# Kernel tuning notes

Measured on AMD Instinct MI355X. Metric: run time of the kernel, lower is better.

Reference implementation:

```python
import jax, jax.numpy as jnp
import numpy as np

S, T, N, D, H, DT = 4, 4, 65536, 128, 128, 128


def setup_inputs() -> dict:
    key = jax.random.key(0)
    ks = jax.random.split(key, 9)
    inv_d = 1.0 / np.sqrt(D)
    inv_h = 1.0 / np.sqrt(H)
    return {
        "states": jax.random.normal(ks[0], (N, D), dtype=jnp.float32),
        "scores": jax.random.uniform(ks[1], (N, 1), dtype=jnp.float32),
        "type_ids": jax.random.randint(ks[2], (N,), 0, S, dtype=jnp.int32),
        "type_matching": jax.random.normal(ks[3], (S, T), dtype=jnp.float32),
        "W1": jax.random.normal(ks[4], (S, T, D, H), dtype=jnp.float32) * inv_d,
        "b1": jnp.zeros((S, T, H), dtype=jnp.float32),
        "W2": jax.random.normal(ks[5], (S, T, H, DT), dtype=jnp.float32) * inv_h,
        "b2": jnp.zeros((S, T, DT), dtype=jnp.float32),
        "C1": jax.random.normal(ks[6], (S, T, D, H), dtype=jnp.float32) * inv_d,
        "c1": jnp.zeros((S, T, H), dtype=jnp.float32),
        "C2": jax.random.normal(ks[7], (S, T, H, 1), dtype=jnp.float32) * inv_h,
        "c2": jnp.zeros((S, T, 1), dtype=jnp.float32),
    }


def reference(states, scores, type_ids, type_matching, W1, b1, W2, b2, C1, c1, C2, c2):
    """Batched MetaphorMorphism.forward with best_match_only=True.

    For each item with source type s: route to t* = argmax sigmoid(type_matching[s]),
    apply mapper MLP (D->H->DT, ReLU), classifier MLP (D->H->1, ReLU, sigmoid),
    new_score = min(score, classifier_out), item_prob = sigmoid(type_matching)[s, t*].
    """
    match_sig = jax.nn.sigmoid(type_matching)          # [S, T]
    best_t = jnp.argmax(type_matching, axis=1)         # [S] (argmax of sigmoid == argmax of logits)
    best_prob = match_sig[jnp.arange(S), best_t]       # [S]

    out_state = jnp.zeros((states.shape[0], W2.shape[-1]), dtype=states.dtype)
    out_score = jnp.zeros_like(scores)
    # loop over the small, fixed set of source types (structurally distinct experts)
    for s in range(S):
        t = best_t[s]
        h = jax.nn.relu(states @ W1[s, t] + b1[s, t])          # [N, H]
        y = h @ W2[s, t] + b2[s, t]                            # [N, DT]
        hc = jax.nn.relu(states @ C1[s, t] + c1[s, t])         # [N, H]
        cls = jax.nn.sigmoid(hc @ C2[s, t] + c2[s, t])         # [N, 1]
        new_score = jnp.minimum(scores, cls)                   # [N, 1]
        m = (type_ids == s)[:, None]
        out_state = jnp.where(m, y, out_state)
        out_score = jnp.where(m, new_score, out_score)
    item_prob = best_prob[type_ids]                            # [N]
    return out_state, out_score, item_prob
```

## Files before the change

### kernel.cpp

```cpp
#include <hip/hip_runtime.h>
#include <hip/hip_bf16.h>

#define Nn 65536

typedef short s16x8 __attribute__((ext_vector_type(8)));
typedef float f32x4 __attribute__((ext_vector_type(4)));

__device__ __forceinline__ unsigned short f2bf(float x) {
    unsigned int u = __float_as_uint(x);
    u += 0x7FFFu + ((u >> 16) & 1u);
    return (unsigned short)(u >> 16);
}

__device__ __forceinline__ int best_t_for(const float* __restrict__ tm, int s, float* mOut) {
    float m = tm[s * 4];
    int am = 0;
    #pragma unroll
    for (int j = 1; j < 4; ++j) {
        float v = tm[s * 4 + j];
        if (v > m) { m = v; am = j; }
    }
    if (mOut) *mOut = m;
    return am;
}

__global__ void k_count(const int* __restrict__ type_ids, const float* __restrict__ tm,
                        int* __restrict__ blockHist, float* __restrict__ out_prob) {
    __shared__ float prob[4];
    __shared__ int hist[4];
    const int tid = threadIdx.x;
    if (tid < 4) {
        hist[tid] = 0;
        float m;
        best_t_for(tm, tid, &m);
        prob[tid] = 1.f / (1.f + expf(-m));
    }
    __syncthreads();
    const int gid = blockIdx.x * 256 + tid;
    int4 ids = ((const int4*)type_ids)[gid];
    float4 p;
    p.x = prob[ids.x]; p.y = prob[ids.y]; p.z = prob[ids.z]; p.w = prob[ids.w];
    ((float4*)out_prob)[gid] = p;
    const int lane = tid & 63;
    int idarr[4] = {ids.x, ids.y, ids.z, ids.w};
    #pragma unroll
    for (int j = 0; j < 4; ++j) {
        #pragma unroll
        for (int sv = 0; sv < 4; ++sv) {
            unsigned long long m = __ballot(idarr[j] == sv);
            if (lane == 0 && m) atomicAdd(&hist[sv], __popcll(m));
        }
    }
    __syncthreads();
    if (tid < 4) blockHist[blockIdx.x * 4 + tid] = hist[tid];
}

__global__ void k_scatter(const int* __restrict__ type_ids, const int* __restrict__ blockHist,
                          int* __restrict__ buckets, int* __restrict__ counts) {
    __shared__ int histAll[256];
    __shared__ int off[4];
    const int tid = threadIdx.x;
    histAll[tid] = blockHist[tid];
    __syncthreads();
    if (tid < 4) {
        int ex = 0, tot = 0;
        for (int b = 0; b < 64; ++b) {
            int v = histAll[b * 4 + tid];
            if (b < (int)blockIdx.x) ex += v;
            tot += v;
        }
        off[tid] = ex;
        if (blockIdx.x == 0) counts[tid] = tot;
    }
    __syncthreads();
    const int gid = blockIdx.x * 256 + tid;
    int4 ids = ((const int4*)type_ids)[gid];
    const int base = gid * 4;
    int idarr[4] = {ids.x, ids.y, ids.z, ids.w};
    #pragma unroll
    for (int j = 0; j < 4; ++j) {
        int sv = idarr[j];
        int pos = atomicAdd(&off[sv], 1);
        buckets[sv * Nn + pos] = base + j;
    }
}

__global__ void k_convert(const float* __restrict__ W1, const float* __restrict__ W2,
                          const float* __restrict__ C1, const float* __restrict__ tm,
                          unsigned short* __restrict__ wbf) {
    int idx = blockIdx.x * 256 + threadIdx.x;
    int mat = idx >> 14;
    int e = idx & 16383;
    int s = mat / 3, w = mat % 3;
    int t = best_t_for(tm, s, nullptr);
    int row = e >> 7, col = e & 127;
    const float* src = (w == 0) ? W1 : (w == 1) ? W2 : C1;
    float v = src[((s * 4 + t) << 14) + col * 128 + row];
    wbf[idx] = f2bf(v);
}

__global__ __launch_bounds__(256, 2) void k_main(
    const float* __restrict__ states, const float* __restrict__ scores,
    const float* __restrict__ b1g, const float* __restrict__ b2g, const float* __restrict__ c1g,
    const float* __restrict__ tm, const float* __restrict__ C2, const float* __restrict__ c2,
    const int* __restrict__ counts, const int* __restrict__ buckets,
    const unsigned short* __restrict__ wbf,
    float* __restrict__ out_state, float* __restrict__ out_score)
{
    __shared__ int gIdx[64];
    __shared__ float C2s[128];
    __shared__ unsigned short Abuf[64 * 136];
    __shared__ unsigned short Hbuf[64 * 136];
    __shared__ unsigned short Wbuf[128 * 136];

    const int s = blockIdx.y;
    const int cnt = counts[s];
    const int rowBase = blockIdx.x << 6;
    if (rowBase >= cnt) return;
    const int valid = (cnt - rowBase < 64) ? (cnt - rowBase) : 64;
    const int t = threadIdx.x;
    const int tt = best_t_for(tm, s, nullptr);
    const int stIdx = s * 4 + tt;

    if (t < 64) gIdx[t] = (t < valid) ? buckets[s * Nn + rowBase + t] : -1;
    if (t >= 128 && t < 256) C2s[t - 128] = C2[stIdx * 128 + (t - 128)];
    __syncthreads();

    {
        int r = t >> 2, q = t & 3;
        int g = gIdx[r];
        unsigned short* dst = &Abuf[r * 136 + q * 32];
        if (g >= 0) {
            const float4* src = (const float4*)(states + (size_t)g * 128 + q * 32);
            #pragma unroll
            for (int i = 0; i < 8; ++i) {
                float4 v = src[i];
                ushort4 o;
                o.x = f2bf(v.x); o.y = f2bf(v.y); o.z = f2bf(v.z); o.w = f2bf(v.w);
                *(ushort4*)(dst + i * 4) = o;
            }
        } else {
            #pragma unroll
            for (int i = 0; i < 8; ++i) *(ushort4*)(dst + i * 4) = ushort4{0, 0, 0, 0};
        }
    }

    const int lane = t & 63;
    const int wv = t >> 6;
    const int m0 = wv << 4;
    const int l15 = lane & 15;
    const int quad = lane >> 4;
    const int kq = quad << 3;

    auto stageW = [&](const unsigned short* src) {
        #pragma unroll
        for (int i = 0; i < 8; ++i) {
            int idx = (t + i * 256) * 8;
            int row = idx >> 7, col = idx & 127;
            s16x8 v = *(const s16x8*)(src + idx);
            *(s16x8*)(&Wbuf[row * 136 + col]) = v;
        }
    };

    auto gemm = [&](const unsigned short* Ab, f32x4 acc[8]) {
        #pragma unroll
        for (int n = 0; n < 8; ++n) acc[n] = f32x4{0.f, 0.f, 0.f, 0.f};
        #pragma unroll
        for (int kk = 0; kk < 4; ++kk) {
            s16x8 af = *(const s16x8*)(Ab + (m0 + l15) * 136 + kk * 32 + kq);
            #pragma unroll
            for (int n = 0; n < 8; ++n) {
                s16x8 bf = *(const s16x8*)(&Wbuf[(n * 16 + l15) * 136 + kk * 32 + kq]);
                acc[n] = __builtin_amdgcn_mfma_f32_16x16x32_bf16(af, bf, acc[n], 0, 0, 0);
            }
        }
    };

    f32x4 acc[8];

    stageW(wbf + (s * 3 + 0) * 16384);
    __syncthreads();
    gemm(Abuf, acc);
    {
        const float* b1p = b1g + stIdx * 128;
        #pragma unroll
        for (int n = 0; n < 8; ++n) {
            int col = n * 16 + l15;
            float bias = b1p[col];
            #pragma unroll
            for (int r = 0; r < 4; ++r) {
                float v = fmaxf(acc[n][r] + bias, 0.f);
                Hbuf[(m0 + quad * 4 + r) * 136 + col] = f2bf(v);
            }
        }
    }
    __syncthreads();

    stageW(wbf + (s * 3 + 1) * 16384);
    __syncthreads();
    gemm(Hbuf, acc);
    {
        int grow[4];
        #pragma unroll
        for (int r = 0; r < 4; ++r) {
            int row = m0 + quad * 4 + r;
            grow[r] = (row < valid) ? gIdx[row] : -1;
        }
        const float* b2p = b2g + stIdx * 128;
        #pragma unroll
        for (int n = 0; n < 8; ++n) {
            int col = n * 16 + l15;
            float bias = b2p[col];
            #pragma unroll
            for (int r = 0; r < 4; ++r) {
                if (grow[r] >= 0) out_state[(size_t)grow[r] * 128 + col] = acc[n][r] + bias;
            }
        }
    }
    __syncthreads();

    stageW(wbf + (s * 3 + 2) * 16384);
    __syncthreads();
    gemm(Abuf, acc);
    {
        const float* c1p = c1g + stIdx * 128;
        float part[4] = {0.f, 0.f, 0.f, 0.f};
        #pragma unroll
        for (int n = 0; n < 8; ++n) {
            int col = n * 16 + l15;
            float cb = c1p[col];
            float cw = C2s[col];
            #pragma unroll
            for (int r = 0; r < 4; ++r) {
                float v = fmaxf(acc[n][r] + cb, 0.f);
                part[r] += v * cw;
            }
        }
        #pragma unroll
        for (int off = 1; off < 16; off <<= 1) {
            #pragma unroll
            for (int r = 0; r < 4; ++r) part[r] += __shfl_xor(part[r], off, 64);
        }
        if (l15 == 0) {
            float c2s = c2[stIdx];
            #pragma unroll
            for (int r = 0; r < 4; ++r) {
                int row = m0 + quad * 4 + r;
                if (row < valid) {
                    int g = gIdx[row];
                    float cls = 1.f / (1.f + expf(-(part[r] + c2s)));
                    out_score[g] = fminf(scores[g], cls);
                }
            }
        }
    }
}

extern "C" void kernel_launch(void* const* d_in, const int* in_sizes, int n_in,
                              void* d_out, int out_size, void* d_ws, size_t ws_size,
                              hipStream_t stream) {
    const float* states = (const float*)d_in[0];
    const float* scores = (const float*)d_in[1];
    const int*   type_ids = (const int*)d_in[2];
    const float* tm = (const float*)d_in[3];
    const float* W1 = (const float*)d_in[4];
    const float* b1 = (const float*)d_in[5];
    const float* W2 = (const float*)d_in[6];
    const float* b2 = (const float*)d_in[7];
    const float* C1 = (const float*)d_in[8];
    const float* c1 = (const float*)d_in[9];
    const float* C2 = (const float*)d_in[10];
    const float* c2 = (const float*)d_in[11];

    char* ws = (char*)d_ws;
    int*   counts    = (int*)(ws + 0);
    int*   blockHist = (int*)(ws + 64);
    int*   buckets   = (int*)(ws + 4096);
    unsigned short* wbf = (unsigned short*)(ws + 1052672);

    float* out_state = (float*)d_out;
    float* out_score = out_state + (size_t)Nn * 128;
    float* out_prob  = out_score + Nn;

    k_count<<<64, 256, 0, stream>>>(type_ids, tm, blockHist, out_prob);
    k_scatter<<<64, 256, 0, stream>>>(type_ids, blockHist, buckets, counts);
    k_convert<<<768, 256, 0, stream>>>(W1, W2, C1, tm, wbf);
    k_main<<<dim3(1024, 4), 256, 0, stream>>>(states, scores, b1, b2, c1,
        tm, C2, c2, counts, buckets, wbf, out_state, out_score);
}
```

Measured before the change: 143.3 us.

## Fuse prep kernels and make main kernel persistent with resident weights and prefetch

```diff
diff --git a/kernel.cpp b/kernel.cpp
--- a/kernel.cpp
+++ b/kernel.cpp
@@ -1,13 +1,14 @@
 #include <hip/hip_runtime.h>
-#include <hip/hip_bf16.h>
+#include <math.h>
 
 #define Nn 65536
 
 typedef short s16x8 __attribute__((ext_vector_type(8)));
 typedef float f32x4 __attribute__((ext_vector_type(4)));
+typedef unsigned int u32;
 
 __device__ __forceinline__ unsigned short f2bf(float x) {
-    unsigned int u = __float_as_uint(x);
+    u32 u = __float_as_uint(x);
     u += 0x7FFFu + ((u >> 16) & 1u);
     return (unsigned short)(u >> 16);
 }
@@ -15,7 +16,7 @@
 __device__ __forceinline__ int best_t_for(const float* __restrict__ tm, int s, float* mOut) {
     float m = tm[s * 4];
     int am = 0;
-    #pragma unroll
+#pragma unroll
     for (int j = 1; j < 4; ++j) {
         float v = tm[s * 4 + j];
         if (v > m) { m = v; am = j; }
@@ -24,82 +25,72 @@
     return am;
 }
 
-__global__ void k_count(const int* __restrict__ type_ids, const float* __restrict__ tm,
-                        int* __restrict__ blockHist, float* __restrict__ out_prob) {
-    __shared__ float prob[4];
-    __shared__ int hist[4];
+#define GLDS16(g, l) __builtin_amdgcn_global_load_lds( \
+    (const __attribute__((address_space(1))) u32*)(g), \
+    (__attribute__((address_space(3))) u32*)(l), 16, 0, 0)
+
+__global__ void k_prep(const int* __restrict__ type_ids, const float* __restrict__ tm,
+                       const float* __restrict__ W1, const float* __restrict__ W2,
+                       const float* __restrict__ C1,
+                       int* __restrict__ counts, int* __restrict__ buckets,
+                       unsigned short* __restrict__ wbf, float* __restrict__ out_prob) {
     const int tid = threadIdx.x;
-    if (tid < 4) {
-        hist[tid] = 0;
-        float m;
-        best_t_for(tm, tid, &m);
-        prob[tid] = 1.f / (1.f + expf(-m));
-    }
-    __syncthreads();
-    const int gid = blockIdx.x * 256 + tid;
-    int4 ids = ((const int4*)type_ids)[gid];
-    float4 p;
-    p.x = prob[ids.x]; p.y = prob[ids.y]; p.z = prob[ids.z]; p.w = prob[ids.w];
-    ((float4*)out_prob)[gid] = p;
-    const int lane = tid & 63;
-    int idarr[4] = {ids.x, ids.y, ids.z, ids.w};
-    #pragma unroll
-    for (int j = 0; j < 4; ++j) {
-        #pragma unroll
-        for (int sv = 0; sv < 4; ++sv) {
-            unsigned long long m = __ballot(idarr[j] == sv);
-            if (lane == 0 && m) atomicAdd(&hist[sv], __popcll(m));
-        }
-    }
-    __syncthreads();
-    if (tid < 4) blockHist[blockIdx.x * 4 + tid] = hist[tid];
-}
-
-__global__ void k_scatter(const int* __restrict__ type_ids, const int* __restrict__ blockHist,
-                          int* __restrict__ buckets, int* __restrict__ counts) {
-    __shared__ int histAll[256];
-    __shared__ int off[4];
-    const int tid = threadIdx.x;
-    histAll[tid] = blockHist[tid];
-    __syncthreads();
-    if (tid < 4) {
-        int ex = 0, tot = 0;
-        for (int b = 0; b < 64; ++b) {
-            int v = histAll[b * 4 + tid];
-            if (b < (int)blockIdx.x) ex += v;
-            tot += v;
-        }
-        off[tid] = ex;
-        if (blockIdx.x == 0) counts[tid] = tot;
-    }
-    __syncthreads();
-    const int gid = blockIdx.x * 256 + tid;
-    int4 ids = ((const int4*)type_ids)[gid];
-    const int base = gid * 4;
-    int idarr[4] = {ids.x, ids.y, ids.z, ids.w};
-    #pragma unroll
-    for (int j = 0; j < 4; ++j) {
-        int sv = idarr[j];
-        int pos = atomicAdd(&off[sv], 1);
-        buckets[sv * Nn + pos] = base + j;
-    }
-}
-
-__global__ void k_convert(const float* __restrict__ W1, const float* __restrict__ W2,
-                          const float* __restrict__ C1, const float* __restrict__ tm,
-                          unsigned short* __restrict__ wbf) {
-    int idx = blockIdx.x * 256 + threadIdx.x;
-    int mat = idx >> 14;
-    int e = idx & 16383;
-    int s = mat / 3, w = mat % 3;
-    int t = best_t_for(tm, s, nullptr);
-    int row = e >> 7, col = e & 127;
-    const float* src = (w == 0) ? W1 : (w == 1) ? W2 : C1;
-    float v = src[((s * 4 + t) << 14) + col * 128 + row];
-    wbf[idx] = f2bf(v);
-}
-
-__global__ __launch_bounds__(256, 2) void k_main(
+    if (blockIdx.x < 64) {
+        __shared__ int hist[4];
+        __shared__ int off[4];
+        __shared__ float prob[4];
+        if (tid < 4) {
+            hist[tid] = 0;
+            float m;
+            best_t_for(tm, tid, &m);
+            prob[tid] = 1.f / (1.f + expf(-m));
+        }
+        __syncthreads();
+        const int gid = blockIdx.x * 256 + tid;
+        int4 ids = ((const int4*)type_ids)[gid];
+        float4 p;
+        p.x = prob[ids.x]; p.y = prob[ids.y]; p.z = prob[ids.z]; p.w = prob[ids.w];
+        ((float4*)out_prob)[gid] = p;
+        const int lane = tid & 63;
+        int idarr[4] = {ids.x, ids.y, ids.z, ids.w};
+#pragma unroll
+        for (int j = 0; j < 4; ++j) {
+#pragma unroll
+            for (int sv = 0; sv < 4; ++sv) {
+                unsigned long long m = __ballot(idarr[j] == sv);
+                if (lane == 0 && m) atomicAdd(&hist[sv], __popcll(m));
+            }
+        }
+        __syncthreads();
+        if (tid < 4) off[tid] = atomicAdd(&counts[tid], hist[tid]);
+        __syncthreads();
+        const int base = gid * 4;
+#pragma unroll
+        for (int j = 0; j < 4; ++j) {
+            int sv = idarr[j];
+            int pos = atomicAdd(&off[sv], 1);
+            buckets[sv * Nn + pos] = base + j;
+        }
+    } else {
+        int u = (blockIdx.x - 64) * 256 + tid;
+        int mat = u >> 11;
+        int rr = u & 2047;
+        int f = rr >> 6, lane = rr & 63;
+        int kk = f >> 3, n8 = f & 7;
+        int q = lane >> 4, l15 = lane & 15;
+        int sm = mat / 3, w = mat - sm * 3;
+        int t = best_t_for(tm, sm, nullptr);
+        const float* src = (w == 0) ? W1 : (w == 1) ? W2 : C1;
+        const float* sp = src + (((sm * 4 + t) << 14) + n8 * 16 + l15);
+        int k0 = kk * 32 + q * 8;
+        s16x8 o;
+#pragma unroll
+        for (int j = 0; j < 8; ++j) o[j] = (short)f2bf(sp[(k0 + j) * 128]);
+        *(s16x8*)(wbf + (size_t)u * 8) = o;
+    }
+}
+
+__global__ __launch_bounds__(256, 1) void k_main(
     const float* __restrict__ states, const float* __restrict__ scores,
     const float* __restrict__ b1g, const float* __restrict__ b2g, const float* __restrict__ c1g,
     const float* __restrict__ tm, const float* __restrict__ C2, const float* __restrict__ c2,
@@ -107,152 +98,185 @@
     const unsigned short* __restrict__ wbf,
     float* __restrict__ out_state, float* __restrict__ out_score)
 {
-    __shared__ int gIdx[64];
+    __shared__ unsigned short Wlds[3 * 16384];
+    __shared__ unsigned short Abuf[2][64 * 136];
+    __shared__ unsigned short Hbuf[64 * 136];
+    __shared__ int gIdxLds[2][64];
     __shared__ float C2s[128];
-    __shared__ unsigned short Abuf[64 * 136];
-    __shared__ unsigned short Hbuf[64 * 136];
-    __shared__ unsigned short Wbuf[128 * 136];
 
     const int s = blockIdx.y;
+    const int bx = blockIdx.x;
     const int cnt = counts[s];
-    const int rowBase = blockIdx.x << 6;
-    if (rowBase >= cnt) return;
-    const int valid = (cnt - rowBase < 64) ? (cnt - rowBase) : 64;
+    const int ntiles = (cnt + 63) >> 6;
+    if (bx >= ntiles) return;
     const int t = threadIdx.x;
     const int tt = best_t_for(tm, s, nullptr);
     const int stIdx = s * 4 + tt;
 
-    if (t < 64) gIdx[t] = (t < valid) ? buckets[s * Nn + rowBase + t] : -1;
-    if (t >= 128 && t < 256) C2s[t - 128] = C2[stIdx * 128 + (t - 128)];
-    __syncthreads();
-
     {
-        int r = t >> 2, q = t & 3;
-        int g = gIdx[r];
-        unsigned short* dst = &Abuf[r * 136 + q * 32];
-        if (g >= 0) {
-            const float4* src = (const float4*)(states + (size_t)g * 128 + q * 32);
-            #pragma unroll
-            for (int i = 0; i < 8; ++i) {
-                float4 v = src[i];
-                ushort4 o;
-                o.x = f2bf(v.x); o.y = f2bf(v.y); o.z = f2bf(v.z); o.w = f2bf(v.w);
-                *(ushort4*)(dst + i * 4) = o;
-            }
-        } else {
-            #pragma unroll
-            for (int i = 0; i < 8; ++i) *(ushort4*)(dst + i * 4) = ushort4{0, 0, 0, 0};
-        }
-    }
+        const unsigned short* src = wbf + (size_t)s * 3 * 16384;
+#pragma unroll
+        for (int i = 0; i < 24; ++i) {
+            GLDS16(src + t * 8 + i * 2048, Wlds + t * 8 + i * 2048);
+        }
+    }
+    if (t >= 128) C2s[t - 128] = C2[stIdx * 128 + (t - 128)];
 
     const int lane = t & 63;
-    const int wv = t >> 6;
-    const int m0 = wv << 4;
+    const int m0 = (t >> 6) << 4;
     const int l15 = lane & 15;
     const int quad = lane >> 4;
     const int kq = quad << 3;
-
-    auto stageW = [&](const unsigned short* src) {
-        #pragma unroll
-        for (int i = 0; i < 8; ++i) {
-            int idx = (t + i * 256) * 8;
-            int row = idx >> 7, col = idx & 127;
-            s16x8 v = *(const s16x8*)(src + idx);
-            *(s16x8*)(&Wbuf[row * 136 + col]) = v;
-        }
-    };
-
-    auto gemm = [&](const unsigned short* Ab, f32x4 acc[8]) {
-        #pragma unroll
+    const int myRow = t >> 2;
+    const int q4 = t & 3;
+
+    const int* bkt = buckets + s * Nn;
+
+    {
+        int gr = bx * 64 + myRow;
+        int rIdxC = (gr < cnt) ? bkt[gr] : -1;
+        if ((t & 3) == 0) gIdxLds[0][myRow] = rIdxC;
+        unsigned short* dst = &Abuf[0][myRow * 136 + q4 * 32];
+        if (rIdxC >= 0) {
+            const float4* sp = (const float4*)(states + (size_t)rIdxC * 128 + q4 * 32);
+            float4 pf0[8];
+#pragma unroll
+            for (int i = 0; i < 8; ++i) pf0[i] = sp[i];
+#pragma unroll
+            for (int i = 0; i < 8; ++i) {
+                ushort4 o;
+                o.x = f2bf(pf0[i].x); o.y = f2bf(pf0[i].y);
+                o.z = f2bf(pf0[i].z); o.w = f2bf(pf0[i].w);
+                *(ushort4*)(dst + i * 4) = o;
+            }
+        } else {
+#pragma unroll
+            for (int i = 0; i < 8; ++i) *(ushort4*)(dst + i * 4) = ushort4{0, 0, 0, 0};
+        }
+    }
+    int rIdxN = -1;
+    if (bx + 64 < ntiles) {
+        int gr = (bx + 64) * 64 + myRow;
+        rIdxN = (gr < cnt) ? bkt[gr] : -1;
+    }
+    __syncthreads();
+
+    auto gemm = [&](const unsigned short* Ab, const unsigned short* Wm, f32x4 acc[8]) {
+#pragma unroll
         for (int n = 0; n < 8; ++n) acc[n] = f32x4{0.f, 0.f, 0.f, 0.f};
-        #pragma unroll
+#pragma unroll
         for (int kk = 0; kk < 4; ++kk) {
             s16x8 af = *(const s16x8*)(Ab + (m0 + l15) * 136 + kk * 32 + kq);
-            #pragma unroll
+#pragma unroll
             for (int n = 0; n < 8; ++n) {
-                s16x8 bf = *(const s16x8*)(&Wbuf[(n * 16 + l15) * 136 + kk * 32 + kq]);
+                s16x8 bf = *(const s16x8*)(Wm + (size_t)((kk * 8 + n) * 64 + lane) * 8);
                 acc[n] = __builtin_amdgcn_mfma_f32_16x16x32_bf16(af, bf, acc[n], 0, 0, 0);
             }
         }
     };
 
     f32x4 acc[8];
-
-    stageW(wbf + (s * 3 + 0) * 16384);
-    __syncthreads();
-    gemm(Abuf, acc);
-    {
-        const float* b1p = b1g + stIdx * 128;
-        #pragma unroll
-        for (int n = 0; n < 8; ++n) {
-            int col = n * 16 + l15;
-            float bias = b1p[col];
-            #pragma unroll
-            for (int r = 0; r < 4; ++r) {
-                float v = fmaxf(acc[n][r] + bias, 0.f);
-                Hbuf[(m0 + quad * 4 + r) * 136 + col] = f2bf(v);
-            }
-        }
-    }
-    __syncthreads();
-
-    stageW(wbf + (s * 3 + 1) * 16384);
-    __syncthreads();
-    gemm(Hbuf, acc);
-    {
-        int grow[4];
-        #pragma unroll
-        for (int r = 0; r < 4; ++r) {
-            int row = m0 + quad * 4 + r;
-            grow[r] = (row < valid) ? gIdx[row] : -1;
-        }
-        const float* b2p = b2g + stIdx * 128;
-        #pragma unroll
-        for (int n = 0; n < 8; ++n) {
-            int col = n * 16 + l15;
-            float bias = b2p[col];
-            #pragma unroll
-            for (int r = 0; r < 4; ++r) {
-                if (grow[r] >= 0) out_state[(size_t)grow[r] * 128 + col] = acc[n][r] + bias;
-            }
-        }
-    }
-    __syncthreads();
-
-    stageW(wbf + (s * 3 + 2) * 16384);
-    __syncthreads();
-    gemm(Abuf, acc);
-    {
-        const float* c1p = c1g + stIdx * 128;
-        float part[4] = {0.f, 0.f, 0.f, 0.f};
-        #pragma unroll
-        for (int n = 0; n < 8; ++n) {
-            int col = n * 16 + l15;
-            float cb = c1p[col];
-            float cw = C2s[col];
-            #pragma unroll
-            for (int r = 0; r < 4; ++r) {
-                float v = fmaxf(acc[n][r] + cb, 0.f);
-                part[r] += v * cw;
-            }
-        }
-        #pragma unroll
-        for (int off = 1; off < 16; off <<= 1) {
-            #pragma unroll
-            for (int r = 0; r < 4; ++r) part[r] += __shfl_xor(part[r], off, 64);
-        }
-        if (l15 == 0) {
-            float c2s = c2[stIdx];
-            #pragma unroll
-            for (int r = 0; r < 4; ++r) {
-                int row = m0 + quad * 4 + r;
-                if (row < valid) {
-                    int g = gIdx[row];
-                    float cls = 1.f / (1.f + expf(-(part[r] + c2s)));
-                    out_score[g] = fminf(scores[g], cls);
-                }
-            }
-        }
+    int cur = 0;
+    for (int tile = bx; tile < ntiles; tile += 64, cur ^= 1) {
+        const int nxt = cur ^ 1;
+        const bool hasNext = (tile + 64) < ntiles;
+
+        gemm(Abuf[cur], Wlds, acc);
+        {
+            const float* b1p = b1g + stIdx * 128;
+#pragma unroll
+            for (int n = 0; n < 8; ++n) {
+                int col = n * 16 + l15;
+                float bias = b1p[col];
+#pragma unroll
+                for (int r = 0; r < 4; ++r) {
+                    float v = fmaxf(acc[n][r] + bias, 0.f);
+                    Hbuf[(m0 + quad * 4 + r) * 136 + col] = f2bf(v);
+                }
+            }
+        }
+        if ((t & 3) == 0) gIdxLds[nxt][myRow] = rIdxN;
+        __syncthreads();
+
+        float4 pf[8];
+        if (hasNext && rIdxN >= 0) {
+            const float4* sp = (const float4*)(states + (size_t)rIdxN * 128 + q4 * 32);
+#pragma unroll
+            for (int i = 0; i < 8; ++i) pf[i] = sp[i];
+        }
+        int rIdxN2 = -1;
+        if (tile + 128 < ntiles) {
+            int gr = (tile + 128) * 64 + myRow;
+            rIdxN2 = (gr < cnt) ? bkt[gr] : -1;
+        }
+
+        gemm(Hbuf, Wlds + 16384, acc);
+        {
+            const float* b2p = b2g + stIdx * 128;
+            int grow[4];
+#pragma unroll
+            for (int r = 0; r < 4; ++r) grow[r] = gIdxLds[cur][m0 + quad * 4 + r];
+#pragma unroll
+            for (int n = 0; n < 8; ++n) {
+                int col = n * 16 + l15;
+                float bias = b2p[col];
+#pragma unroll
+                for (int r = 0; r < 4; ++r) {
+                    if (grow[r] >= 0) out_state[(size_t)grow[r] * 128 + col] = acc[n][r] + bias;
+                }
+            }
+        }
+
+        gemm(Abuf[cur], Wlds + 2 * 16384, acc);
+        {
+            const float* c1p = c1g + stIdx * 128;
+            float part[4] = {0.f, 0.f, 0.f, 0.f};
+#pragma unroll
+            for (int n = 0; n < 8; ++n) {
+                int col = n * 16 + l15;
+                float cb = c1p[col];
+                float cw = C2s[col];
+#pragma unroll
+                for (int r = 0; r < 4; ++r) {
+                    float v = fmaxf(acc[n][r] + cb, 0.f);
+                    part[r] += v * cw;
+                }
+            }
+#pragma unroll
+            for (int off = 1; off < 16; off <<= 1) {
+#pragma unroll
+                for (int r = 0; r < 4; ++r) part[r] += __shfl_xor(part[r], off, 64);
+            }
+            if (l15 == 0) {
+                float c2s = c2[stIdx];
+#pragma unroll
+                for (int r = 0; r < 4; ++r) {
+                    int g = gIdxLds[cur][m0 + quad * 4 + r];
+                    if (g >= 0) {
+                        float cls = 1.f / (1.f + expf(-(part[r] + c2s)));
+                        out_score[g] = fminf(scores[g], cls);
+                    }
+                }
+            }
+        }
+
+        if (hasNext) {
+            unsigned short* dst = &Abuf[nxt][myRow * 136 + q4 * 32];
+            if (rIdxN >= 0) {
+#pragma unroll
+                for (int i = 0; i < 8; ++i) {
+                    ushort4 o;
+                    o.x = f2bf(pf[i].x); o.y = f2bf(pf[i].y);
+                    o.z = f2bf(pf[i].z); o.w = f2bf(pf[i].w);
+                    *(ushort4*)(dst + i * 4) = o;
+                }
+            } else {
+#pragma unroll
+                for (int i = 0; i < 8; ++i) *(ushort4*)(dst + i * 4) = ushort4{0, 0, 0, 0};
+            }
+        }
+        rIdxN = rIdxN2;
+        __syncthreads();
     }
 }
 
@@ -273,18 +297,16 @@
     const float* c2 = (const float*)d_in[11];
 
     char* ws = (char*)d_ws;
-    int*   counts    = (int*)(ws + 0);
-    int*   blockHist = (int*)(ws + 64);
-    int*   buckets   = (int*)(ws + 4096);
+    int*   counts  = (int*)(ws + 0);
+    int*   buckets = (int*)(ws + 4096);
     unsigned short* wbf = (unsigned short*)(ws + 1052672);
 
     float* out_state = (float*)d_out;
     float* out_score = out_state + (size_t)Nn * 128;
     float* out_prob  = out_score + Nn;
 
-    k_count<<<64, 256, 0, stream>>>(type_ids, tm, blockHist, out_prob);
-    k_scatter<<<64, 256, 0, stream>>>(type_ids, blockHist, buckets, counts);
-    k_convert<<<768, 256, 0, stream>>>(W1, W2, C1, tm, wbf);
-    k_main<<<dim3(1024, 4), 256, 0, stream>>>(states, scores, b1, b2, c1,
+    hipMemsetAsync(counts, 0, 16, stream);
+    k_prep<<<160, 256, 0, stream>>>(type_ids, tm, W1, W2, C1, counts, buckets, wbf, out_prob);
+    k_main<<<dim3(64, 4), 256, 0, stream>>>(states, scores, b1, b2, c1,
         tm, C2, c2, counts, buckets, wbf, out_state, out_score);
 }
```

Result: faster. 131.9 us (-7.9%).
